# Kernel optimization log

Hardware: AMD Instinct MI355X
Metric: run time of the kernel (lower is better)

The kernel has to match this reference:

```python
import jax, jax.numpy as jnp
import numpy as np

B, LC, LE, H, V = 128, 256, 257, 512, 128
PAD = 0  # padding_token_index


def lstm_cell(x, h, c, Wih, Whh, b):
    # torch LSTMCell gate order: i, f, g, o
    g = x @ Wih.T + h @ Whh.T + b
    i, f, gg, o = jnp.split(g, 4, axis=-1)
    c = jax.nn.sigmoid(f) * c + jax.nn.sigmoid(i) * jnp.tanh(gg)
    h = jax.nn.sigmoid(o) * jnp.tanh(c)
    return h, c


def setup_inputs() -> dict:
    key = jax.random.key(0)
    ks = jax.random.split(key, 32)
    p = lambda k, shape: jax.random.normal(k, shape, jnp.float32) * 0.05
    d = {
        'C_idx': jax.random.randint(ks[0], (B, LC), 0, V, dtype=jnp.int32),
        'E_idx': jax.random.randint(ks[1], (B, LE), 0, V, dtype=jnp.int32),
        'C_pad': jnp.zeros((B, LC), dtype=bool),
        'enc_Wih_f': p(ks[2], (4 * H, V)),
        'enc_Whh_f': p(ks[3], (4 * H, H)),
        'enc_b_f': p(ks[4], (4 * H,)),
        'enc_Wih_b': p(ks[5], (4 * H, V)),
        'enc_Whh_b': p(ks[6], (4 * H, H)),
        'enc_b_b': p(ks[7], (4 * H,)),
        'dec_Wih': p(ks[8], (4 * H, H + V)),
        'dec_Whh': p(ks[9], (4 * H, H)),
        'dec_b': p(ks[10], (4 * H,)),
        'Wh': p(ks[11], (H, 2 * H)),
        'Wc': p(ks[12], (H, 2 * H)),
        'Wattn': p(ks[13], (H, 2 * H)),
        'Wout': p(ks[14], (H, 3 * H)),
        'Wvocab': p(ks[15], (V, H)),
        'pg_ctx': p(ks[16], (2 * H,)),
        'pg_in': p(ks[17], (V + H,)),
        'pg_h': p(ks[18], (H,)),
        'pg_c': p(ks[19], (H,)),
        'pg_b': p(ks[20], (1,)),
    }
    return d


def _forward(C_idx, E_idx, C_pad, enc_Wih_f, enc_Whh_f, enc_b_f, enc_Wih_b, enc_Whh_b, enc_b_b,
             dec_Wih, dec_Whh, dec_b, Wh, Wc, Wattn, Wout, Wvocab,
             pg_ctx, pg_in, pg_h, pg_c, pg_b):
    C = jax.nn.one_hot(C_idx, V, dtype=jnp.float32)      # [B,LC,V]
    E_emb = jax.nn.one_hot(E_idx, V, dtype=jnp.float32)  # [B,LE,V]
    z = jnp.zeros((B, H), jnp.float32)

    xs = jnp.swapaxes(C, 0, 1)  # [LC,B,V]

    def enc_fwd(carry, x):
        h, c = lstm_cell(x, carry[0], carry[1], enc_Wih_f, enc_Whh_f, enc_b_f)
        return (h, c), h

    def enc_bwd(carry, x):
        h, c = lstm_cell(x, carry[0], carry[1], enc_Wih_b, enc_Whh_b, enc_b_b)
        return (h, c), h

    (hf, cf), Hf = jax.lax.scan(enc_fwd, (z, z), xs)
    (hb, cb), Hb = jax.lax.scan(enc_bwd, (z, z), xs[::-1])
    Hb = Hb[::-1]
    enc = jnp.swapaxes(jnp.concatenate([Hf, Hb], axis=-1), 0, 1)  # [B,LC,2H]

    # decoder init state from final encoder states (fwd;bwd concat)
    h0 = jnp.concatenate([hf, hb], axis=-1) @ Wh.T
    c0 = jnp.concatenate([cf, cb], axis=-1) @ Wc.T

    enc_proj = enc @ Wattn.T  # [B,LC,H]

    def step(carry, x_emb):
        h, c, prev_out = carry
        nin = jnp.concatenate([x_emb, prev_out], axis=1)  # [B,V+H]
        h, c = lstm_cell(nin, h, c, dec_Wih, dec_Whh, dec_b)
        scores = jnp.einsum('blh,bh->bl', enc_proj, h)
        scores = jnp.where(C_pad, -jnp.inf, scores)
        attn = jax.nn.softmax(scores, axis=1)             # [B,LC]
        ctx = jnp.einsum('bl,blh->bh', attn, enc)         # [B,2H]
        t_out = jnp.tanh(jnp.concatenate([h, ctx], axis=1) @ Wout.T)  # [B,H]
        gen = jax.nn.softmax(t_out @ Wvocab.T, axis=1)    # [B,V]
        p_gen = jax.nn.sigmoid(ctx @ pg_ctx + nin @ pg_in + h @ pg_h + c @ pg_c + pg_b[0])[:, None]
        copy_p = attn * (1.0 - p_gen)
        out = jax.vmap(lambda o, idx, a: o.at[idx].add(a))(gen * p_gen, C_idx, copy_p)
        return (h, c, t_out), out

    xs2 = jnp.swapaxes(E_emb[:, :LE - 1], 0, 1)  # teacher inputs, step 0 = start token
    _, preds = jax.lax.scan(step, (h0, c0, z), xs2)
    preds = jnp.swapaxes(preds, 0, 1)  # [B,LE-1,V]

    tgt = E_idx[:, 1:]
    nll = -jnp.take_along_axis(jnp.log(preds), tgt[..., None], axis=2)[..., 0]
    return jnp.where(tgt == PAD, 0.0, nll)  # [B,LE-1], reduction='none'


def reference(C_idx, E_idx, C_pad, enc_Wih_f, enc_Whh_f, enc_b_f, enc_Wih_b, enc_Whh_b, enc_b_b,
              dec_Wih, dec_Whh, dec_b, Wh, Wc, Wattn, Wout, Wvocab,
              pg_ctx, pg_in, pg_h, pg_c, pg_b):
    return _forward(C_idx, E_idx, C_pad, enc_Wih_f, enc_Whh_f, enc_b_f, enc_Wih_b, enc_Whh_b, enc_b_b,
                    dec_Wih, dec_Whh, dec_b, Wh, Wc, Wattn, Wout, Wvocab,
                    pg_ctx, pg_in, pg_h, pg_c, pg_b)
```

## Files before the change

### kernel.cpp

```cpp
#include <hip/hip_runtime.h>

static constexpr int B_   = 128;
static constexpr int LC_  = 256;
static constexpr int LE_  = 257;
static constexpr int H_   = 512;
static constexpr size_t HB_ = (size_t)512 * 128;

static constexpr size_t OFF_ENC    = 0;
static constexpr size_t SZ_ENC     = (size_t)128 * 256 * 1024 * 2;
static constexpr size_t OFF_WIHFT  = OFF_ENC + SZ_ENC;
static constexpr size_t OFF_WIHBT  = OFF_WIHFT + (size_t)128 * 2048 * 4;
static constexpr size_t OFF_XDEC   = OFF_WIHBT + (size_t)128 * 2048 * 4;
static constexpr size_t OFF_WATTNT = OFF_XDEC + (size_t)128 * 2048 * 4;
static constexpr size_t OFF_HENC   = OFF_WATTNT + (size_t)1024 * 512 * 4;
static constexpr size_t OFF_CENC   = OFF_HENC + 4 * HB_ * 4;
static constexpr size_t OFF_HDEC   = OFF_CENC + 2 * HB_ * 4;
static constexpr size_t OFF_CDEC   = OFF_HDEC + 2 * HB_ * 4;
static constexpr size_t OFF_TOUT   = OFF_CDEC + HB_ * 4;
static constexpr size_t OFF_U      = OFF_TOUT + 2 * HB_ * 4;
static constexpr size_t OFF_CTX    = OFF_U + (size_t)1024 * 128 * 4;
static constexpr size_t OFF_SC     = OFF_CTX + (size_t)1024 * 128 * 4;
static constexpr size_t OFF_MD     = OFF_SC + (size_t)128 * 256 * 4;

__device__ __forceinline__ float sigm(float x) { return 1.f / (1.f + expf(-x)); }
__device__ __forceinline__ unsigned short f2bf(float f) {
  unsigned u = __float_as_uint(f);
  u += 0x7fffu + ((u >> 16) & 1u);
  return (unsigned short)(u >> 16);
}
__device__ __forceinline__ float bfl(unsigned w) { return __uint_as_float(w << 16); }
__device__ __forceinline__ float bfh(unsigned w) { return __uint_as_float(w & 0xffff0000u); }

__global__ __launch_bounds__(256) void k_pre(const float* __restrict__ wihF,
                                             const float* __restrict__ wihB,
                                             const float* __restrict__ dWih,
                                             const float* __restrict__ Wattn,
                                             float* __restrict__ ws) {
  float* WT_F = (float*)((char*)ws + OFF_WIHFT);
  float* WT_B = (float*)((char*)ws + OFF_WIHBT);
  float* XD   = (float*)((char*)ws + OFF_XDEC);
  float* WAT  = (float*)((char*)ws + OFF_WATTNT);
  int stride = gridDim.x * blockDim.x;
  int i0 = blockIdx.x * blockDim.x + threadIdx.x;
  for (int x = i0; x < 128 * 2048; x += stride) {
    int v = x >> 11, n = x & 2047;
    WT_F[x] = wihF[n * 128 + v];
    WT_B[x] = wihB[n * 128 + v];
    XD[x]   = dWih[n * 640 + v];
  }
  for (int x = i0; x < 1024 * 512; x += stride) {
    int j = x >> 9, i2 = x & 511;
    WAT[x] = Wattn[i2 * 1024 + j];
  }
}

__global__ __launch_bounds__(512) void k_enc(const float* __restrict__ WhhF,
                                             const float* __restrict__ WhhB,
                                             const float* __restrict__ bF,
                                             const float* __restrict__ bB,
                                             const int* __restrict__ C_idx,
                                             float* __restrict__ ws, int t) {
  int p = blockIdx.x * 512 + threadIdx.x;
  int b = p & 127;
  int j = (p >> 7) & 511;
  int dir = p >> 16;
  int jj = __builtin_amdgcn_readfirstlane(j);
  int dd = __builtin_amdgcn_readfirstlane(dir);
  const float* Whh  = dd ? WhhB : WhhF;
  const float* bias = dd ? bB : bF;
  const float* WihT = (const float*)((char*)ws + (dd ? OFF_WIHBT : OFF_WIHFT));
  int l = dd ? (LC_ - 1 - t) : t;
  int cidx = C_idx[b * LC_ + l];
  int par = t & 1;
  const float* hp = (const float*)((char*)ws + OFF_HENC) + (size_t)(dir * 2 + (par ^ 1)) * HB_ + b;

  const float* w0 = Whh + (size_t)jj * 512;
  const float* w1 = Whh + (size_t)(512 + jj) * 512;
  const float* w2 = Whh + (size_t)(1024 + jj) * 512;
  const float* w3 = Whh + (size_t)(1536 + jj) * 512;
  float a0 = bias[jj]        + WihT[(size_t)cidx * 2048 + jj];
  float a1 = bias[512 + jj]  + WihT[(size_t)cidx * 2048 + 512 + jj];
  float a2 = bias[1024 + jj] + WihT[(size_t)cidx * 2048 + 1024 + jj];
  float a3 = bias[1536 + jj] + WihT[(size_t)cidx * 2048 + 1536 + jj];
  for (int k = 0; k < 512; k += 4) {
    float4 W0 = *(const float4*)(w0 + k);
    float4 W1 = *(const float4*)(w1 + k);
    float4 W2 = *(const float4*)(w2 + k);
    float4 W3 = *(const float4*)(w3 + k);
    float h0 = hp[(size_t)k * 128], h1 = hp[(size_t)(k + 1) * 128];
    float h2 = hp[(size_t)(k + 2) * 128], h3 = hp[(size_t)(k + 3) * 128];
    a0 += W0.x * h0 + W0.y * h1 + W0.z * h2 + W0.w * h3;
    a1 += W1.x * h0 + W1.y * h1 + W1.z * h2 + W1.w * h3;
    a2 += W2.x * h0 + W2.y * h1 + W2.z * h2 + W2.w * h3;
    a3 += W3.x * h0 + W3.y * h1 + W3.z * h2 + W3.w * h3;
  }
  float ig = sigm(a0), fg = sigm(a1), gg = tanhf(a2), og = sigm(a3);
  float* cp = (float*)((char*)ws + OFF_CENC) + (size_t)dir * HB_ + (size_t)j * 128 + b;
  float c = fg * (*cp) + ig * gg;
  *cp = c;
  float h = og * tanhf(c);
  ((float*)((char*)ws + OFF_HENC))[(size_t)(dir * 2 + par) * HB_ + (size_t)j * 128 + b] = h;
  ((unsigned short*)((char*)ws + OFF_ENC))[((size_t)b * LC_ + l) * 1024 + dir * 512 + j] = f2bf(h);
}

__global__ __launch_bounds__(512) void k_h0c0(const float* __restrict__ Wh,
                                              const float* __restrict__ Wc,
                                              float* __restrict__ ws) {
  int p = blockIdx.x * 512 + threadIdx.x;
  int b = p & 127;
  int n = (p >> 7) & 511;
  int sel = p >> 16;
  int nn = __builtin_amdgcn_readfirstlane(n);
  int ss = __builtin_amdgcn_readfirstlane(sel);
  const float* W = (ss ? Wc : Wh) + (size_t)nn * 1024;
  const float* hf = (const float*)((char*)ws + OFF_HENC) + (size_t)1 * HB_ + b;
  const float* hb = (const float*)((char*)ws + OFF_HENC) + (size_t)3 * HB_ + b;
  float acc = 0.f;
  for (int k = 0; k < 512; k += 4) {
    float4 Wa = *(const float4*)(W + k);
    float4 Wb = *(const float4*)(W + 512 + k);
    acc += Wa.x * hf[(size_t)k * 128] + Wa.y * hf[(size_t)(k + 1) * 128]
         + Wa.z * hf[(size_t)(k + 2) * 128] + Wa.w * hf[(size_t)(k + 3) * 128];
    acc += Wb.x * hb[(size_t)k * 128] + Wb.y * hb[(size_t)(k + 1) * 128]
         + Wb.z * hb[(size_t)(k + 2) * 128] + Wb.w * hb[(size_t)(k + 3) * 128];
  }
  float* dst = (float*)((char*)ws + (ss ? OFF_CDEC : OFF_HDEC));
  dst[(size_t)n * 128 + b] = acc;
}

__device__ void s4_body(float* __restrict__ ws, float* __restrict__ out,
                        const float* __restrict__ Wvocab, const int* __restrict__ E_idx,
                        const int* __restrict__ C_idx, int b, int t) {
  __shared__ float to[516];
  __shared__ float lgp[128][4];
  __shared__ float lg[128];
  __shared__ float red2[8];
  __shared__ float mx_s[2];
  int tau = threadIdx.x;
  const float* TO = (const float*)((char*)ws + OFF_TOUT) + (size_t)(t & 1) * HB_;
  to[tau + (tau >> 7)] = TO[(size_t)tau * 128 + b];
  __syncthreads();
  int v = tau >> 2, seg = tau & 3;
  const float* wv = Wvocab + (size_t)v * 512 + seg * 128;
  const float* tp = &to[seg * 128 + seg];
  float part = 0.f;
#pragma unroll 8
  for (int i = 0; i < 128; ++i) part += tp[i] * wv[i];
  lgp[v][seg] = part;
  __syncthreads();
  if (tau < 128) lg[tau] = lgp[tau][0] + lgp[tau][1] + lgp[tau][2] + lgp[tau][3];
  __syncthreads();
  if (tau < 64) {
    float m2 = fmaxf(lg[tau], lg[tau + 64]);
    for (int o = 32; o; o >>= 1) m2 = fmaxf(m2, __shfl_xor(m2, o));
    float e = expf(lg[tau] - m2) + expf(lg[tau + 64] - m2);
    for (int o = 32; o; o >>= 1) e += __shfl_xor(e, o);
    if (tau == 0) { mx_s[0] = m2; mx_s[1] = e; }
  }
  const float* MD = (const float*)((char*)ws + OFF_MD);
  float Mb = MD[b], Db = MD[128 + b], pg = MD[256 + b];
  int tgt = E_idx[b * LE_ + t];
  float cm = 0.f;
  if (tau < 256) {
    float s = ((const float*)((char*)ws + OFF_SC))[b * 256 + tau];
    if (C_idx[b * 256 + tau] == tgt) cm = expf(s - Mb);
  }
  for (int o = 32; o; o >>= 1) cm += __shfl_xor(cm, o);
  if ((tau & 63) == 0) red2[tau >> 6] = cm;
  __syncthreads();
  if (tau == 0) {
    float mass = (red2[0] + red2[1] + red2[2] + red2[3]) / Db;
    float gen_tgt = expf(lg[tgt] - mx_s[0]) / mx_s[1];
    float prob = pg * gen_tgt + (1.f - pg) * mass;
    out[b * 256 + (t - 1)] = (tgt == 0) ? 0.f : -logf(prob);
  }
}

__global__ __launch_bounds__(512) void k_dgates(const float* __restrict__ dWih,
                                                const float* __restrict__ dWhh,
                                                const float* __restrict__ db,
                                                const float* __restrict__ Wvocab,
                                                const int* __restrict__ E_idx,
                                                const int* __restrict__ C_idx,
                                                float* __restrict__ ws,
                                                float* __restrict__ out, int t) {
  int tau = threadIdx.x;
  if (blockIdx.x >= 256) {
    if (t > 0) s4_body(ws, out, Wvocab, E_idx, C_idx, blockIdx.x - 256, t);
    return;
  }
  __shared__ float part[4][256];
  int kh = tau >> 8, q = tau & 255;
  int pp = blockIdx.x * 256 + q;
  int b = pp & 127, j = pp >> 7;
  int jj = __builtin_amdgcn_readfirstlane(j);
  int pr = t & 1;
  float a0 = 0.f, a1 = 0.f, a2 = 0.f, a3 = 0.f;
  if (kh == 0) {
    const float* w0 = dWih + (size_t)jj * 640 + 128;
    const float* w1 = dWih + (size_t)(512 + jj) * 640 + 128;
    const float* w2 = dWih + (size_t)(1024 + jj) * 640 + 128;
    const float* w3 = dWih + (size_t)(1536 + jj) * 640 + 128;
    const float* po = (const float*)((char*)ws + OFF_TOUT) + (size_t)pr * HB_ + b;
    for (int k = 0; k < 512; k += 4) {
      float4 W0 = *(const float4*)(w0 + k);
      float4 W1 = *(const float4*)(w1 + k);
      float4 W2 = *(const float4*)(w2 + k);
      float4 W3 = *(const float4*)(w3 + k);
      float h0 = po[(size_t)k * 128], h1 = po[(size_t)(k + 1) * 128];
      float h2 = po[(size_t)(k + 2) * 128], h3 = po[(size_t)(k + 3) * 128];
      a0 += W0.x * h0 + W0.y * h1 + W0.z * h2 + W0.w * h3;
      a1 += W1.x * h0 + W1.y * h1 + W1.z * h2 + W1.w * h3;
      a2 += W2.x * h0 + W2.y * h1 + W2.z * h2 + W2.w * h3;
      a3 += W3.x * h0 + W3.y * h1 + W3.z * h2 + W3.w * h3;
    }
  } else {
    const float* w0 = dWhh + (size_t)jj * 512;
    const float* w1 = dWhh + (size_t)(512 + jj) * 512;
    const float* w2 = dWhh + (size_t)(1024 + jj) * 512;
    const float* w3 = dWhh + (size_t)(1536 + jj) * 512;
    const float* hp = (const float*)((char*)ws + OFF_HDEC) + (size_t)pr * HB_ + b;
    for (int k = 0; k < 512; k += 4) {
      float4 W0 = *(const float4*)(w0 + k);
      float4 W1 = *(const float4*)(w1 + k);
      float4 W2 = *(const float4*)(w2 + k);
      float4 W3 = *(const float4*)(w3 + k);
      float h0 = hp[(size_t)k * 128], h1 = hp[(size_t)(k + 1) * 128];
      float h2 = hp[(size_t)(k + 2) * 128], h3 = hp[(size_t)(k + 3) * 128];
      a0 += W0.x * h0 + W0.y * h1 + W0.z * h2 + W0.w * h3;
      a1 += W1.x * h0 + W1.y * h1 + W1.z * h2 + W1.w * h3;
      a2 += W2.x * h0 + W2.y * h1 + W2.z * h2 + W2.w * h3;
      a3 += W3.x * h0 + W3.y * h1 + W3.z * h2 + W3.w * h3;
    }
    part[0][q] = a0; part[1][q] = a1; part[2][q] = a2; part[3][q] = a3;
  }
  __syncthreads();
  if (kh == 0) {
    int xid = E_idx[b * LE_ + t];
    const float* xg = (const float*)((char*)ws + OFF_XDEC) + (size_t)xid * 2048;
    float g0 = a0 + part[0][q] + db[jj]        + xg[jj];
    float g1 = a1 + part[1][q] + db[512 + jj]  + xg[512 + jj];
    float g2 = a2 + part[2][q] + db[1024 + jj] + xg[1024 + jj];
    float g3 = a3 + part[3][q] + db[1536 + jj] + xg[1536 + jj];
    float ig = sigm(g0), fg = sigm(g1), gg = tanhf(g2), og = sigm(g3);
    float* cp = (float*)((char*)ws + OFF_CDEC) + (size_t)j * 128 + b;
    float c = fg * (*cp) + ig * gg;
    *cp = c;
    ((float*)((char*)ws + OFF_HDEC))[(size_t)(pr ^ 1) * HB_ + (size_t)j * 128 + b] = og * tanhf(c);
  }
}

__global__ __launch_bounds__(512) void k_u(const float* __restrict__ unused,
                                           float* __restrict__ ws, int t) {
  int p = blockIdx.x * 512 + threadIdx.x;
  int b = p & 127, j = p >> 7;
  int jj = __builtin_amdgcn_readfirstlane(j);
  const float* w = (const float*)((char*)ws + OFF_WATTNT) + (size_t)jj * 512;
  const float* hp = (const float*)((char*)ws + OFF_HDEC) + (size_t)((t & 1) ^ 1) * HB_ + b;
  float acc = 0.f;
  for (int k = 0; k < 512; k += 4) {
    float4 W = *(const float4*)(w + k);
    acc += W.x * hp[(size_t)k * 128] + W.y * hp[(size_t)(k + 1) * 128]
         + W.z * hp[(size_t)(k + 2) * 128] + W.w * hp[(size_t)(k + 3) * 128];
  }
  ((float*)((char*)ws + OFF_U))[(size_t)j * 128 + b] = acc;
}

__global__ __launch_bounds__(512) void k_attn(const float* __restrict__ pg_ctx,
                                              const float* __restrict__ pg_in,
                                              const float* __restrict__ pg_h,
                                              const float* __restrict__ pg_c,
                                              const float* __restrict__ pg_b,
                                              const int* __restrict__ E_idx,
                                              const unsigned char* __restrict__ C_pad,
                                              float* __restrict__ ws, int t) {
  __shared__ unsigned short tile[65536];
  __shared__ float u_lds[1032];
  __shared__ float scp[64][9];
  __shared__ float p_lds[64];
  __shared__ float sred[8];
  __shared__ float bc[2];
  int b = blockIdx.x, tau = threadIdx.x;
  int pr = t & 1;
  const float* U = (const float*)((char*)ws + OFF_U);
  u_lds[tau + (tau >> 7)] = U[(size_t)tau * 128 + b];
  {
    int x2 = tau + 512;
    u_lds[x2 + (x2 >> 7)] = U[(size_t)x2 * 128 + b];
  }
  float M = -3.0e38f, D = 0.f, c0 = 0.f, c1 = 0.f;
  const uint4* encb = (const uint4*)((char*)ws + OFF_ENC + (size_t)b * LC_ * 1024 * 2);
  float* SC = (float*)((char*)ws + OFF_SC);
  int l = tau >> 3, seg = tau & 7;
  for (int lb = 0; lb < 4; ++lb) {
    const uint4* src = encb + (size_t)lb * 64 * 128;
#pragma unroll
    for (int it = 0; it < 16; ++it) {
      int fl = it * 512 + tau;
      int r = fl >> 7, cb = fl & 127;
      ((uint4*)tile)[(r << 7) + (cb ^ (r & 7))] = src[fl];
    }
    __syncthreads();
    float acc = 0.f;
#pragma unroll
    for (int ibv = 0; ibv < 16; ++ibv) {
      int blk = (seg * 16 + ibv) ^ (l & 7);
      const uint4 wv = *(const uint4*)&tile[(l << 10) + (blk << 3)];
      const float* up = &u_lds[seg * 128 + ibv * 8 + seg];
      acc += bfl(wv.x) * up[0] + bfh(wv.x) * up[1];
      acc += bfl(wv.y) * up[2] + bfh(wv.y) * up[3];
      acc += bfl(wv.z) * up[4] + bfh(wv.z) * up[5];
      acc += bfl(wv.w) * up[6] + bfh(wv.w) * up[7];
    }
    scp[l][seg] = acc;
    __syncthreads();
    if (tau < 64) {
      float s = scp[tau][0] + scp[tau][1] + scp[tau][2] + scp[tau][3]
              + scp[tau][4] + scp[tau][5] + scp[tau][6] + scp[tau][7];
      int gl = lb * 64 + tau;
      if (C_pad[b * LC_ + gl]) s = -3.0e38f;
      SC[b * 256 + gl] = s;
      float m = s;
      for (int o = 32; o; o >>= 1) m = fmaxf(m, __shfl_xor(m, o));
      float Mn = fmaxf(M, m);
      float pv = expf(s - Mn);
      p_lds[tau] = pv;
      float ds = pv;
      for (int o = 32; o; o >>= 1) ds += __shfl_xor(ds, o);
      if (tau == 0) { bc[0] = m; bc[1] = ds; }
    }
    __syncthreads();
    float Mn = fmaxf(M, bc[0]);
    float scale = expf(M - Mn);
    D = D * scale + bc[1];
    c0 *= scale; c1 *= scale;
    M = Mn;
    {
      int cb0 = tau >> 3, e0 = tau & 7;
      int cb1 = (tau + 512) >> 3;
#pragma unroll 8
      for (int l2 = 0; l2 < 64; ++l2) {
        float pv = p_lds[l2];
        float v0 = bfl((unsigned)tile[(l2 << 10) + (((cb0 ^ (l2 & 7)) << 3) | e0)]);
        float v1 = bfl((unsigned)tile[(l2 << 10) + (((cb1 ^ (l2 & 7)) << 3) | e0)]);
        c0 += pv * v0; c1 += pv * v1;
      }
    }
    __syncthreads();
  }
  float inv = 1.f / D;
  float x0 = c0 * inv, x1 = c1 * inv;
  float* CTX = (float*)((char*)ws + OFF_CTX);
  CTX[(size_t)tau * 128 + b] = x0;
  CTX[(size_t)(tau + 512) * 128 + b] = x1;
  float pp = x0 * pg_ctx[tau] + x1 * pg_ctx[tau + 512];
  pp += ((const float*)((char*)ws + OFF_HDEC))[(size_t)(pr ^ 1) * HB_ + (size_t)tau * 128 + b] * pg_h[tau];
  pp += ((const float*)((char*)ws + OFF_CDEC))[(size_t)tau * 128 + b] * pg_c[tau];
  pp += ((const float*)((char*)ws + OFF_TOUT))[(size_t)pr * HB_ + (size_t)tau * 128 + b] * pg_in[128 + tau];
  for (int o = 32; o; o >>= 1) pp += __shfl_xor(pp, o);
  if ((tau & 63) == 0) sred[tau >> 6] = pp;
  __syncthreads();
  if (tau == 0) {
    float s = sred[0] + sred[1] + sred[2] + sred[3] + sred[4] + sred[5] + sred[6] + sred[7];
    int xid = E_idx[b * LE_ + t];
    s += pg_in[xid] + pg_b[0];
    float* MD = (float*)((char*)ws + OFF_MD);
    MD[256 + b] = sigm(s);
    MD[b] = M;
    MD[128 + b] = D;
  }
}

__global__ __launch_bounds__(512) void k_wout(const float* __restrict__ Wout,
                                              float* __restrict__ ws, int t) {
  __shared__ float part[256];
  int tau = threadIdx.x;
  int kh = tau >> 8, q = tau & 255;
  int pp = blockIdx.x * 256 + q;
  int b = pp & 127, n = pp >> 7;
  int nn = __builtin_amdgcn_readfirstlane(n);
  int pr = t & 1;
  float acc = 0.f;
  if (kh == 0) {
    const float* w = Wout + (size_t)nn * 1536;
    const float* hp = (const float*)((char*)ws + OFF_HDEC) + (size_t)(pr ^ 1) * HB_ + b;
    for (int k = 0; k < 512; k += 4) {
      float4 W = *(const float4*)(w + k);
      acc += W.x * hp[(size_t)k * 128] + W.y * hp[(size_t)(k + 1) * 128]
           + W.z * hp[(size_t)(k + 2) * 128] + W.w * hp[(size_t)(k + 3) * 128];
    }
  } else {
    const float* w = Wout + (size_t)nn * 1536 + 512;
    const float* cp = (const float*)((char*)ws + OFF_CTX) + b;
    for (int k = 0; k < 1024; k += 4) {
      float4 W = *(const float4*)(w + k);
      acc += W.x * cp[(size_t)k * 128] + W.y * cp[(size_t)(k + 1) * 128]
           + W.z * cp[(size_t)(k + 2) * 128] + W.w * cp[(size_t)(k + 3) * 128];
    }
    part[q] = acc;
  }
  __syncthreads();
  if (kh == 0) {
    float s = acc + part[q];
    ((float*)((char*)ws + OFF_TOUT))[(size_t)(pr ^ 1) * HB_ + (size_t)n * 128 + b] = tanhf(s);
  }
}

__global__ __launch_bounds__(512) void k_final(const float* __restrict__ Wvocab,
                                               const int* __restrict__ E_idx,
                                               const int* __restrict__ C_idx,
                                               float* __restrict__ ws,
                                               float* __restrict__ out) {
  s4_body(ws, out, Wvocab, E_idx, C_idx, blockIdx.x, 256);
}

extern "C" void kernel_launch(void* const* d_in, const int* in_sizes, int n_in,
                              void* d_out, int out_size, void* d_ws, size_t ws_size,
                              hipStream_t stream) {
  (void)in_sizes; (void)n_in; (void)out_size; (void)ws_size;
  const int* C_idx = (const int*)d_in[0];
  const int* E_idx = (const int*)d_in[1];
  const unsigned char* C_pad = (const unsigned char*)d_in[2];
  const float* eWihF = (const float*)d_in[3];
  const float* eWhhF = (const float*)d_in[4];
  const float* ebF   = (const float*)d_in[5];
  const float* eWihB = (const float*)d_in[6];
  const float* eWhhB = (const float*)d_in[7];
  const float* ebB   = (const float*)d_in[8];
  const float* dWih  = (const float*)d_in[9];
  const float* dWhh  = (const float*)d_in[10];
  const float* db    = (const float*)d_in[11];
  const float* Wh    = (const float*)d_in[12];
  const float* Wc    = (const float*)d_in[13];
  const float* Wattn = (const float*)d_in[14];
  const float* Wout  = (const float*)d_in[15];
  const float* Wvoc  = (const float*)d_in[16];
  const float* pgc   = (const float*)d_in[17];
  const float* pgi   = (const float*)d_in[18];
  const float* pgh   = (const float*)d_in[19];
  const float* pgcc  = (const float*)d_in[20];
  const float* pgb   = (const float*)d_in[21];
  float* ws = (float*)d_ws;
  float* out = (float*)d_out;

  hipMemsetAsync((char*)d_ws + OFF_HENC, 0, 6 * HB_ * 4, stream);
  hipMemsetAsync((char*)d_ws + OFF_TOUT, 0, 2 * HB_ * 4, stream);

  k_pre<<<512, 256, 0, stream>>>(eWihF, eWihB, dWih, Wattn, ws);
  for (int t = 0; t < 256; ++t)
    k_enc<<<256, 512, 0, stream>>>(eWhhF, eWhhB, ebF, ebB, C_idx, ws, t);
  k_h0c0<<<256, 512, 0, stream>>>(Wh, Wc, ws);
  for (int t = 0; t < 256; ++t) {
    k_dgates<<<384, 512, 0, stream>>>(dWih, dWhh, db, Wvoc, E_idx, C_idx, ws, out, t);
    k_u<<<256, 512, 0, stream>>>(nullptr, ws, t);
    k_attn<<<128, 512, 0, stream>>>(pgc, pgi, pgh, pgcc, pgb, E_idx, C_pad, ws, t);
    k_wout<<<256, 512, 0, stream>>>(Wout, ws, t);
  }
  k_final<<<128, 512, 0, stream>>>(Wvoc, E_idx, C_idx, ws, out);
}
```

Before: 34.11 ms.

## Fuse all per-step kernels into one persistent cooperative kernel with grid barriers

Replaces about 1300 separate kernel launches (encoder steps, decoder gates, attention projection, attention, output projection) with one cooperative persistent kernel of 256 blocks. The phases are separated by a hierarchical atomic grid barrier. The change is meant to remove per-launch overhead and the gaps between launches in the long sequential recurrence. It also changes the bf16 encoder-output layout to a swizzled tiled form, likely to suit attention LDS tiles, and double-buffers the score and MD buffers so the loss computation can overlap with attention. The risks are barrier correctness and lost parallelism in phases that previously used more blocks, such as the former 384-block dgates launch.

```diff
diff --git a/kernel.cpp b/kernel.cpp
--- a/kernel.cpp
+++ b/kernel.cpp
@@ -1,26 +1,43 @@
 #include <hip/hip_runtime.h>
 
-static constexpr int B_   = 128;
-static constexpr int LC_  = 256;
-static constexpr int LE_  = 257;
-static constexpr int H_   = 512;
-static constexpr size_t HB_ = (size_t)512 * 128;
+static constexpr int NBLK = 256;
+static constexpr int NTHR = 512;
+static constexpr size_t HB = (size_t)512 * 128;
 
 static constexpr size_t OFF_ENC    = 0;
-static constexpr size_t SZ_ENC     = (size_t)128 * 256 * 1024 * 2;
-static constexpr size_t OFF_WIHFT  = OFF_ENC + SZ_ENC;
-static constexpr size_t OFF_WIHBT  = OFF_WIHFT + (size_t)128 * 2048 * 4;
-static constexpr size_t OFF_XDEC   = OFF_WIHBT + (size_t)128 * 2048 * 4;
-static constexpr size_t OFF_WATTNT = OFF_XDEC + (size_t)128 * 2048 * 4;
-static constexpr size_t OFF_HENC   = OFF_WATTNT + (size_t)1024 * 512 * 4;
-static constexpr size_t OFF_CENC   = OFF_HENC + 4 * HB_ * 4;
-static constexpr size_t OFF_HDEC   = OFF_CENC + 2 * HB_ * 4;
-static constexpr size_t OFF_CDEC   = OFF_HDEC + 2 * HB_ * 4;
-static constexpr size_t OFF_TOUT   = OFF_CDEC + HB_ * 4;
-static constexpr size_t OFF_U      = OFF_TOUT + 2 * HB_ * 4;
-static constexpr size_t OFF_CTX    = OFF_U + (size_t)1024 * 128 * 4;
-static constexpr size_t OFF_SC     = OFF_CTX + (size_t)1024 * 128 * 4;
-static constexpr size_t OFF_MD     = OFF_SC + (size_t)128 * 256 * 4;
+static constexpr size_t OFF_WIHFT  = 67108864;
+static constexpr size_t OFF_WIHBT  = 68157440;
+static constexpr size_t OFF_XDEC   = 69206016;
+static constexpr size_t OFF_WATTNT = 70254592;
+static constexpr size_t OFF_HENC   = 72351744;
+static constexpr size_t OFF_CENC   = 73400320;
+static constexpr size_t OFF_HDEC   = 73924608;
+static constexpr size_t OFF_CDEC   = 74448896;
+static constexpr size_t OFF_TOUT   = 74711040;
+static constexpr size_t OFF_U      = 75235328;
+static constexpr size_t OFF_CTX    = 75759616;
+static constexpr size_t OFF_SC     = 76283904;
+static constexpr size_t OFF_MD     = 76546048;
+static constexpr size_t OFF_BAR    = 76550144;
+
+static constexpr int SM_TILE = 0;
+static constexpr int SM_U    = 131072;
+static constexpr int SM_SCP  = 135232;
+static constexpr int SM_PLDS = 137536;
+static constexpr int SM_BC   = 137792;
+static constexpr int SM_RED  = 137824;
+static constexpr int SM_PVP  = 137856;
+static constexpr int SM_SIZE = 150208;
+
+struct KP {
+  const int* C_idx; const int* E_idx; const unsigned char* C_pad;
+  const float* eWihF; const float* eWhhF; const float* ebF;
+  const float* eWihB; const float* eWhhB; const float* ebB;
+  const float* dWih;  const float* dWhh;  const float* db;
+  const float* Wh; const float* Wc; const float* Wattn; const float* Wout; const float* Wvoc;
+  const float* pgc; const float* pgi; const float* pgh; const float* pgcc; const float* pgb;
+  char* wsb; float* out;
+};
 
 __device__ __forceinline__ float sigm(float x) { return 1.f / (1.f + expf(-x)); }
 __device__ __forceinline__ unsigned short f2bf(float f) {
@@ -31,48 +48,61 @@
 __device__ __forceinline__ float bfl(unsigned w) { return __uint_as_float(w << 16); }
 __device__ __forceinline__ float bfh(unsigned w) { return __uint_as_float(w & 0xffff0000u); }
 
-__global__ __launch_bounds__(256) void k_pre(const float* __restrict__ wihF,
-                                             const float* __restrict__ wihB,
-                                             const float* __restrict__ dWih,
-                                             const float* __restrict__ Wattn,
-                                             float* __restrict__ ws) {
-  float* WT_F = (float*)((char*)ws + OFF_WIHFT);
-  float* WT_B = (float*)((char*)ws + OFF_WIHBT);
-  float* XD   = (float*)((char*)ws + OFF_XDEC);
-  float* WAT  = (float*)((char*)ws + OFF_WATTNT);
-  int stride = gridDim.x * blockDim.x;
-  int i0 = blockIdx.x * blockDim.x + threadIdx.x;
+__device__ __forceinline__ void gbar(int* bar, int bid) {
+  __syncthreads();
+  if (threadIdx.x == 0) {
+    __threadfence();
+    int* gen = bar + 32;
+    int g = __hip_atomic_load(gen, __ATOMIC_RELAXED, __HIP_MEMORY_SCOPE_AGENT);
+    int* gc = bar + 64 + (bid >> 4) * 32;
+    if (__hip_atomic_fetch_add(gc, 1, __ATOMIC_ACQ_REL, __HIP_MEMORY_SCOPE_AGENT) == 15) {
+      __hip_atomic_store(gc, 0, __ATOMIC_RELAXED, __HIP_MEMORY_SCOPE_AGENT);
+      if (__hip_atomic_fetch_add(bar, 1, __ATOMIC_ACQ_REL, __HIP_MEMORY_SCOPE_AGENT) == 15) {
+        __hip_atomic_store(bar, 0, __ATOMIC_RELAXED, __HIP_MEMORY_SCOPE_AGENT);
+        __hip_atomic_store(gen, g + 1, __ATOMIC_RELEASE, __HIP_MEMORY_SCOPE_AGENT);
+      }
+    }
+    while (__hip_atomic_load(gen, __ATOMIC_ACQUIRE, __HIP_MEMORY_SCOPE_AGENT) == g)
+      __builtin_amdgcn_s_sleep(2);
+    __threadfence();
+  }
+  __syncthreads();
+}
+
+__device__ void pre_phase(const KP& P, int bid, int tau) {
+  float* WT_F = (float*)(P.wsb + OFF_WIHFT);
+  float* WT_B = (float*)(P.wsb + OFF_WIHBT);
+  float* XD   = (float*)(P.wsb + OFF_XDEC);
+  float* WAT  = (float*)(P.wsb + OFF_WATTNT);
+  int i0 = bid * NTHR + tau;
+  int stride = NBLK * NTHR;
   for (int x = i0; x < 128 * 2048; x += stride) {
     int v = x >> 11, n = x & 2047;
-    WT_F[x] = wihF[n * 128 + v];
-    WT_B[x] = wihB[n * 128 + v];
-    XD[x]   = dWih[n * 640 + v];
+    WT_F[x] = P.eWihF[n * 128 + v];
+    WT_B[x] = P.eWihB[n * 128 + v];
+    XD[x]   = P.dWih[n * 640 + v];
   }
   for (int x = i0; x < 1024 * 512; x += stride) {
     int j = x >> 9, i2 = x & 511;
-    WAT[x] = Wattn[i2 * 1024 + j];
-  }
-}
-
-__global__ __launch_bounds__(512) void k_enc(const float* __restrict__ WhhF,
-                                             const float* __restrict__ WhhB,
-                                             const float* __restrict__ bF,
-                                             const float* __restrict__ bB,
-                                             const int* __restrict__ C_idx,
-                                             float* __restrict__ ws, int t) {
-  int p = blockIdx.x * 512 + threadIdx.x;
+    WAT[x] = P.Wattn[i2 * 1024 + j];
+  }
+}
+
+__device__ void enc_phase(const KP& P, int bid, int tau, int t) {
+  char* wsb = P.wsb;
+  int p = bid * NTHR + tau;
   int b = p & 127;
   int j = (p >> 7) & 511;
   int dir = p >> 16;
   int jj = __builtin_amdgcn_readfirstlane(j);
   int dd = __builtin_amdgcn_readfirstlane(dir);
-  const float* Whh  = dd ? WhhB : WhhF;
-  const float* bias = dd ? bB : bF;
-  const float* WihT = (const float*)((char*)ws + (dd ? OFF_WIHBT : OFF_WIHFT));
-  int l = dd ? (LC_ - 1 - t) : t;
-  int cidx = C_idx[b * LC_ + l];
+  const float* Whh  = dd ? P.eWhhB : P.eWhhF;
+  const float* bias = dd ? P.ebB : P.ebF;
+  const float* WihT = (const float*)(wsb + (dd ? OFF_WIHBT : OFF_WIHFT));
+  int l = dd ? (255 - t) : t;
+  int cidx = P.C_idx[b * 256 + l];
   int par = t & 1;
-  const float* hp = (const float*)((char*)ws + OFF_HENC) + (size_t)(dir * 2 + (par ^ 1)) * HB_ + b;
+  const float* hp = (const float*)(wsb + OFF_HENC) + (size_t)(dir * 2 + (par ^ 1)) * HB + b;
 
   const float* w0 = Whh + (size_t)jj * 512;
   const float* w1 = Whh + (size_t)(512 + jj) * 512;
@@ -95,113 +125,57 @@
     a3 += W3.x * h0 + W3.y * h1 + W3.z * h2 + W3.w * h3;
   }
   float ig = sigm(a0), fg = sigm(a1), gg = tanhf(a2), og = sigm(a3);
-  float* cp = (float*)((char*)ws + OFF_CENC) + (size_t)dir * HB_ + (size_t)j * 128 + b;
+  float* cp = (float*)(wsb + OFF_CENC) + (size_t)dir * HB + (size_t)j * 128 + b;
   float c = fg * (*cp) + ig * gg;
   *cp = c;
   float h = og * tanhf(c);
-  ((float*)((char*)ws + OFF_HENC))[(size_t)(dir * 2 + par) * HB_ + (size_t)j * 128 + b] = h;
-  ((unsigned short*)((char*)ws + OFF_ENC))[((size_t)b * LC_ + l) * 1024 + dir * 512 + j] = f2bf(h);
-}
-
-__global__ __launch_bounds__(512) void k_h0c0(const float* __restrict__ Wh,
-                                              const float* __restrict__ Wc,
-                                              float* __restrict__ ws) {
-  int p = blockIdx.x * 512 + threadIdx.x;
+  ((float*)(wsb + OFF_HENC))[(size_t)(dir * 2 + par) * HB + (size_t)j * 128 + b] = h;
+  int f = dir * 512 + j;
+  int cb = f >> 3, e = f & 7;
+  int r = l & 63, lbt = l >> 6;
+  size_t idx = (size_t)b * 262144 + (size_t)lbt * 65536 + ((size_t)r << 10) + ((size_t)(cb ^ (r & 7)) << 3) + e;
+  ((unsigned short*)(wsb + OFF_ENC))[idx] = f2bf(h);
+}
+
+__device__ void h0c0_phase(const KP& P, int bid, int tau) {
+  char* wsb = P.wsb;
+  int p = bid * NTHR + tau;
   int b = p & 127;
   int n = (p >> 7) & 511;
   int sel = p >> 16;
   int nn = __builtin_amdgcn_readfirstlane(n);
   int ss = __builtin_amdgcn_readfirstlane(sel);
-  const float* W = (ss ? Wc : Wh) + (size_t)nn * 1024;
-  const float* hf = (const float*)((char*)ws + OFF_HENC) + (size_t)1 * HB_ + b;
-  const float* hb = (const float*)((char*)ws + OFF_HENC) + (size_t)3 * HB_ + b;
+  const float* W = (ss ? P.Wc : P.Wh) + (size_t)nn * 1024;
+  const float* af = (const float*)(wsb + (ss ? OFF_CENC : OFF_HENC + HB * 4)) + b;
+  const float* ab = (const float*)(wsb + (ss ? OFF_CENC + HB * 4 : OFF_HENC + 3 * HB * 4)) + b;
   float acc = 0.f;
   for (int k = 0; k < 512; k += 4) {
     float4 Wa = *(const float4*)(W + k);
     float4 Wb = *(const float4*)(W + 512 + k);
-    acc += Wa.x * hf[(size_t)k * 128] + Wa.y * hf[(size_t)(k + 1) * 128]
-         + Wa.z * hf[(size_t)(k + 2) * 128] + Wa.w * hf[(size_t)(k + 3) * 128];
-    acc += Wb.x * hb[(size_t)k * 128] + Wb.y * hb[(size_t)(k + 1) * 128]
-         + Wb.z * hb[(size_t)(k + 2) * 128] + Wb.w * hb[(size_t)(k + 3) * 128];
-  }
-  float* dst = (float*)((char*)ws + (ss ? OFF_CDEC : OFF_HDEC));
+    acc += Wa.x * af[(size_t)k * 128] + Wa.y * af[(size_t)(k + 1) * 128]
+         + Wa.z * af[(size_t)(k + 2) * 128] + Wa.w * af[(size_t)(k + 3) * 128];
+    acc += Wb.x * ab[(size_t)k * 128] + Wb.y * ab[(size_t)(k + 1) * 128]
+         + Wb.z * ab[(size_t)(k + 2) * 128] + Wb.w * ab[(size_t)(k + 3) * 128];
+  }
+  float* dst = (float*)(wsb + (ss ? OFF_CDEC : OFF_HDEC));
   dst[(size_t)n * 128 + b] = acc;
 }
 
-__device__ void s4_body(float* __restrict__ ws, float* __restrict__ out,
-                        const float* __restrict__ Wvocab, const int* __restrict__ E_idx,
-                        const int* __restrict__ C_idx, int b, int t) {
-  __shared__ float to[516];
-  __shared__ float lgp[128][4];
-  __shared__ float lg[128];
-  __shared__ float red2[8];
-  __shared__ float mx_s[2];
-  int tau = threadIdx.x;
-  const float* TO = (const float*)((char*)ws + OFF_TOUT) + (size_t)(t & 1) * HB_;
-  to[tau + (tau >> 7)] = TO[(size_t)tau * 128 + b];
-  __syncthreads();
-  int v = tau >> 2, seg = tau & 3;
-  const float* wv = Wvocab + (size_t)v * 512 + seg * 128;
-  const float* tp = &to[seg * 128 + seg];
-  float part = 0.f;
-#pragma unroll 8
-  for (int i = 0; i < 128; ++i) part += tp[i] * wv[i];
-  lgp[v][seg] = part;
-  __syncthreads();
-  if (tau < 128) lg[tau] = lgp[tau][0] + lgp[tau][1] + lgp[tau][2] + lgp[tau][3];
-  __syncthreads();
-  if (tau < 64) {
-    float m2 = fmaxf(lg[tau], lg[tau + 64]);
-    for (int o = 32; o; o >>= 1) m2 = fmaxf(m2, __shfl_xor(m2, o));
-    float e = expf(lg[tau] - m2) + expf(lg[tau + 64] - m2);
-    for (int o = 32; o; o >>= 1) e += __shfl_xor(e, o);
-    if (tau == 0) { mx_s[0] = m2; mx_s[1] = e; }
-  }
-  const float* MD = (const float*)((char*)ws + OFF_MD);
-  float Mb = MD[b], Db = MD[128 + b], pg = MD[256 + b];
-  int tgt = E_idx[b * LE_ + t];
-  float cm = 0.f;
-  if (tau < 256) {
-    float s = ((const float*)((char*)ws + OFF_SC))[b * 256 + tau];
-    if (C_idx[b * 256 + tau] == tgt) cm = expf(s - Mb);
-  }
-  for (int o = 32; o; o >>= 1) cm += __shfl_xor(cm, o);
-  if ((tau & 63) == 0) red2[tau >> 6] = cm;
-  __syncthreads();
-  if (tau == 0) {
-    float mass = (red2[0] + red2[1] + red2[2] + red2[3]) / Db;
-    float gen_tgt = expf(lg[tgt] - mx_s[0]) / mx_s[1];
-    float prob = pg * gen_tgt + (1.f - pg) * mass;
-    out[b * 256 + (t - 1)] = (tgt == 0) ? 0.f : -logf(prob);
-  }
-}
-
-__global__ __launch_bounds__(512) void k_dgates(const float* __restrict__ dWih,
-                                                const float* __restrict__ dWhh,
-                                                const float* __restrict__ db,
-                                                const float* __restrict__ Wvocab,
-                                                const int* __restrict__ E_idx,
-                                                const int* __restrict__ C_idx,
-                                                float* __restrict__ ws,
-                                                float* __restrict__ out, int t) {
-  int tau = threadIdx.x;
-  if (blockIdx.x >= 256) {
-    if (t > 0) s4_body(ws, out, Wvocab, E_idx, C_idx, blockIdx.x - 256, t);
-    return;
-  }
-  __shared__ float part[4][256];
+__device__ void dgates_phase(const KP& P, char* smem, int bid, int tau, int t) {
+  char* wsb = P.wsb;
+  float (*part)[256] = (float(*)[256])smem;
   int kh = tau >> 8, q = tau & 255;
-  int pp = blockIdx.x * 256 + q;
+  int pp = bid * 256 + q;
   int b = pp & 127, j = pp >> 7;
   int jj = __builtin_amdgcn_readfirstlane(j);
   int pr = t & 1;
   float a0 = 0.f, a1 = 0.f, a2 = 0.f, a3 = 0.f;
   if (kh == 0) {
-    const float* w0 = dWih + (size_t)jj * 640 + 128;
-    const float* w1 = dWih + (size_t)(512 + jj) * 640 + 128;
-    const float* w2 = dWih + (size_t)(1024 + jj) * 640 + 128;
-    const float* w3 = dWih + (size_t)(1536 + jj) * 640 + 128;
-    const float* po = (const float*)((char*)ws + OFF_TOUT) + (size_t)pr * HB_ + b;
+    const float* w0 = P.dWih + (size_t)jj * 640 + 128;
+    const float* w1 = P.dWih + (size_t)(512 + jj) * 640 + 128;
+    const float* w2 = P.dWih + (size_t)(1024 + jj) * 640 + 128;
+    const float* w3 = P.dWih + (size_t)(1536 + jj) * 640 + 128;
+    const float* po = (const float*)(wsb + OFF_TOUT) + (size_t)pr * HB + b;
     for (int k = 0; k < 512; k += 4) {
       float4 W0 = *(const float4*)(w0 + k);
       float4 W1 = *(const float4*)(w1 + k);
@@ -215,11 +189,11 @@
       a3 += W3.x * h0 + W3.y * h1 + W3.z * h2 + W3.w * h3;
     }
   } else {
-    const float* w0 = dWhh + (size_t)jj * 512;
-    const float* w1 = dWhh + (size_t)(512 + jj) * 512;
-    const float* w2 = dWhh + (size_t)(1024 + jj) * 512;
-    const float* w3 = dWhh + (size_t)(1536 + jj) * 512;
-    const float* hp = (const float*)((char*)ws + OFF_HDEC) + (size_t)pr * HB_ + b;
+    const float* w0 = P.dWhh + (size_t)jj * 512;
+    const float* w1 = P.dWhh + (size_t)(512 + jj) * 512;
+    const float* w2 = P.dWhh + (size_t)(1024 + jj) * 512;
+    const float* w3 = P.dWhh + (size_t)(1536 + jj) * 512;
+    const float* hp = (const float*)(wsb + OFF_HDEC) + (size_t)pr * HB + b;
     for (int k = 0; k < 512; k += 4) {
       float4 W0 = *(const float4*)(w0 + k);
       float4 W1 = *(const float4*)(w1 + k);
@@ -236,90 +210,85 @@
   }
   __syncthreads();
   if (kh == 0) {
-    int xid = E_idx[b * LE_ + t];
-    const float* xg = (const float*)((char*)ws + OFF_XDEC) + (size_t)xid * 2048;
-    float g0 = a0 + part[0][q] + db[jj]        + xg[jj];
-    float g1 = a1 + part[1][q] + db[512 + jj]  + xg[512 + jj];
-    float g2 = a2 + part[2][q] + db[1024 + jj] + xg[1024 + jj];
-    float g3 = a3 + part[3][q] + db[1536 + jj] + xg[1536 + jj];
+    int xid = P.E_idx[b * 257 + t];
+    const float* xg = (const float*)(wsb + OFF_XDEC) + (size_t)xid * 2048;
+    float g0 = a0 + part[0][q] + P.db[jj]        + xg[jj];
+    float g1 = a1 + part[1][q] + P.db[512 + jj]  + xg[512 + jj];
+    float g2 = a2 + part[2][q] + P.db[1024 + jj] + xg[1024 + jj];
+    float g3 = a3 + part[3][q] + P.db[1536 + jj] + xg[1536 + jj];
     float ig = sigm(g0), fg = sigm(g1), gg = tanhf(g2), og = sigm(g3);
-    float* cp = (float*)((char*)ws + OFF_CDEC) + (size_t)j * 128 + b;
+    float* cp = (float*)(wsb + OFF_CDEC) + (size_t)j * 128 + b;
     float c = fg * (*cp) + ig * gg;
     *cp = c;
-    ((float*)((char*)ws + OFF_HDEC))[(size_t)(pr ^ 1) * HB_ + (size_t)j * 128 + b] = og * tanhf(c);
-  }
-}
-
-__global__ __launch_bounds__(512) void k_u(const float* __restrict__ unused,
-                                           float* __restrict__ ws, int t) {
-  int p = blockIdx.x * 512 + threadIdx.x;
+    ((float*)(wsb + OFF_HDEC))[(size_t)(pr ^ 1) * HB + (size_t)j * 128 + b] = og * tanhf(c);
+  }
+}
+
+__device__ void u_phase(const KP& P, int bid, int tau, int t) {
+  char* wsb = P.wsb;
+  int p = bid * NTHR + tau;
   int b = p & 127, j = p >> 7;
   int jj = __builtin_amdgcn_readfirstlane(j);
-  const float* w = (const float*)((char*)ws + OFF_WATTNT) + (size_t)jj * 512;
-  const float* hp = (const float*)((char*)ws + OFF_HDEC) + (size_t)((t & 1) ^ 1) * HB_ + b;
+  const float* w = (const float*)(wsb + OFF_WATTNT) + (size_t)jj * 512;
+  const float* hp = (const float*)(wsb + OFF_HDEC) + (size_t)((t & 1) ^ 1) * HB + b;
   float acc = 0.f;
   for (int k = 0; k < 512; k += 4) {
     float4 W = *(const float4*)(w + k);
     acc += W.x * hp[(size_t)k * 128] + W.y * hp[(size_t)(k + 1) * 128]
          + W.z * hp[(size_t)(k + 2) * 128] + W.w * hp[(size_t)(k + 3) * 128];
   }
-  ((float*)((char*)ws + OFF_U))[(size_t)j * 128 + b] = acc;
-}
-
-__global__ __launch_bounds__(512) void k_attn(const float* __restrict__ pg_ctx,
-                                              const float* __restrict__ pg_in,
-                                              const float* __restrict__ pg_h,
-                                              const float* __restrict__ pg_c,
-                                              const float* __restrict__ pg_b,
-                                              const int* __restrict__ E_idx,
-                                              const unsigned char* __restrict__ C_pad,
-                                              float* __restrict__ ws, int t) {
-  __shared__ unsigned short tile[65536];
-  __shared__ float u_lds[1032];
-  __shared__ float scp[64][9];
-  __shared__ float p_lds[64];
-  __shared__ float sred[8];
-  __shared__ float bc[2];
-  int b = blockIdx.x, tau = threadIdx.x;
+  ((float*)(wsb + OFF_U))[(size_t)j * 128 + b] = acc;
+}
+
+__device__ void attn_phase(const KP& P, char* smem, int b, int tau, int t) {
+  char* wsb = P.wsb;
+  unsigned short* tile = (unsigned short*)(smem + SM_TILE);
+  uint4* tile4 = (uint4*)(smem + SM_TILE);
+  float* u_lds = (float*)(smem + SM_U);
+  float (*scp)[9] = (float(*)[9])(smem + SM_SCP);
+  float* p_lds = (float*)(smem + SM_PLDS);
+  float* bc = (float*)(smem + SM_BC);
+  float* red = (float*)(smem + SM_RED);
+  float* pvp = (float*)(smem + SM_PVP);
   int pr = t & 1;
-  const float* U = (const float*)((char*)ws + OFF_U);
+  const float* U = (const float*)(wsb + OFF_U);
   u_lds[tau + (tau >> 7)] = U[(size_t)tau * 128 + b];
-  {
-    int x2 = tau + 512;
-    u_lds[x2 + (x2 >> 7)] = U[(size_t)x2 * 128 + b];
-  }
-  float M = -3.0e38f, D = 0.f, c0 = 0.f, c1 = 0.f;
-  const uint4* encb = (const uint4*)((char*)ws + OFF_ENC + (size_t)b * LC_ * 1024 * 2);
-  float* SC = (float*)((char*)ws + OFF_SC);
+  { int x2 = tau + 512; u_lds[x2 + (x2 >> 7)] = U[(size_t)x2 * 128 + b]; }
+  float M = -3.0e38f, D = 0.f;
+  float acc[8];
+#pragma unroll
+  for (int e = 0; e < 8; ++e) acc[e] = 0.f;
+  const uint4* encb = (const uint4*)(wsb + OFF_ENC + (size_t)b * 524288);
+  float* SCp = (float*)(wsb + OFF_SC) + (size_t)pr * 128 * 256;
   int l = tau >> 3, seg = tau & 7;
+  int fg = tau & 127, rs = tau >> 7;
   for (int lb = 0; lb < 4; ++lb) {
-    const uint4* src = encb + (size_t)lb * 64 * 128;
+    const uint4* src = encb + (size_t)lb * 8192;
 #pragma unroll
     for (int it = 0; it < 16; ++it) {
       int fl = it * 512 + tau;
-      int r = fl >> 7, cb = fl & 127;
-      ((uint4*)tile)[(r << 7) + (cb ^ (r & 7))] = src[fl];
+      tile4[fl] = src[fl];
     }
     __syncthreads();
-    float acc = 0.f;
+    float sacc = 0.f;
 #pragma unroll
     for (int ibv = 0; ibv < 16; ++ibv) {
       int blk = (seg * 16 + ibv) ^ (l & 7);
-      const uint4 wv = *(const uint4*)&tile[(l << 10) + (blk << 3)];
+      const uint4 wv = tile4[(l << 7) + blk];
       const float* up = &u_lds[seg * 128 + ibv * 8 + seg];
-      acc += bfl(wv.x) * up[0] + bfh(wv.x) * up[1];
-      acc += bfl(wv.y) * up[2] + bfh(wv.y) * up[3];
-      acc += bfl(wv.z) * up[4] + bfh(wv.z) * up[5];
-      acc += bfl(wv.w) * up[6] + bfh(wv.w) * up[7];
-    }
-    scp[l][seg] = acc;
+      sacc += bfl(wv.x) * up[0] + bfh(wv.x) * up[1];
+      sacc += bfl(wv.y) * up[2] + bfh(wv.y) * up[3];
+      sacc += bfl(wv.z) * up[4] + bfh(wv.z) * up[5];
+      sacc += bfl(wv.w) * up[6] + bfh(wv.w) * up[7];
+    }
+    scp[l][seg] = sacc;
     __syncthreads();
     if (tau < 64) {
       float s = scp[tau][0] + scp[tau][1] + scp[tau][2] + scp[tau][3]
               + scp[tau][4] + scp[tau][5] + scp[tau][6] + scp[tau][7];
       int gl = lb * 64 + tau;
-      if (C_pad[b * LC_ + gl]) s = -3.0e38f;
-      SC[b * 256 + gl] = s;
+      if (P.C_pad[b * 256 + gl]) s = -3.0e38f;
+      SCp[b * 256 + gl] = s;
       float m = s;
       for (int o = 32; o; o >>= 1) m = fmaxf(m, __shfl_xor(m, o));
       float Mn = fmaxf(M, m);
@@ -333,65 +302,140 @@
     float Mn = fmaxf(M, bc[0]);
     float scale = expf(M - Mn);
     D = D * scale + bc[1];
-    c0 *= scale; c1 *= scale;
     M = Mn;
-    {
-      int cb0 = tau >> 3, e0 = tau & 7;
-      int cb1 = (tau + 512) >> 3;
+#pragma unroll
+    for (int e = 0; e < 8; ++e) acc[e] *= scale;
+    int base = rs * 16;
+#pragma unroll
+    for (int l2i = 0; l2i < 16; ++l2i) {
+      int l2 = base + l2i;
+      float pv = p_lds[l2];
+      const uint4 wv = tile4[(l2 << 7) + (fg ^ (l2 & 7))];
+      acc[0] += pv * bfl(wv.x); acc[1] += pv * bfh(wv.x);
+      acc[2] += pv * bfl(wv.y); acc[3] += pv * bfh(wv.y);
+      acc[4] += pv * bfl(wv.z); acc[5] += pv * bfh(wv.z);
+      acc[6] += pv * bfl(wv.w); acc[7] += pv * bfh(wv.w);
+    }
+    __syncthreads();
+  }
+  if (rs > 0) {
+    float4* dst = (float4*)(pvp + (rs - 1) * 1024 + fg * 8);
+    dst[0] = make_float4(acc[0], acc[1], acc[2], acc[3]);
+    dst[1] = make_float4(acc[4], acc[5], acc[6], acc[7]);
+  }
+  __syncthreads();
+  if (rs == 0) {
+    float inv = 1.f / D;
+    float* CTX = (float*)(wsb + OFF_CTX);
+    float4 q0 = ((float4*)(pvp + fg * 8))[0],        q1 = ((float4*)(pvp + fg * 8))[1];
+    float4 r0 = ((float4*)(pvp + 1024 + fg * 8))[0], r1 = ((float4*)(pvp + 1024 + fg * 8))[1];
+    float4 s0 = ((float4*)(pvp + 2048 + fg * 8))[0], s1 = ((float4*)(pvp + 2048 + fg * 8))[1];
+    float x0 = (acc[0] + q0.x + r0.x + s0.x) * inv;
+    float x1 = (acc[1] + q0.y + r0.y + s0.y) * inv;
+    float x2 = (acc[2] + q0.z + r0.z + s0.z) * inv;
+    float x3 = (acc[3] + q0.w + r0.w + s0.w) * inv;
+    float x4 = (acc[4] + q1.x + r1.x + s1.x) * inv;
+    float x5 = (acc[5] + q1.y + r1.y + s1.y) * inv;
+    float x6 = (acc[6] + q1.z + r1.z + s1.z) * inv;
+    float x7 = (acc[7] + q1.w + r1.w + s1.w) * inv;
+    ((float4*)(pvp + fg * 8))[0] = make_float4(x0, x1, x2, x3);
+    ((float4*)(pvp + fg * 8))[1] = make_float4(x4, x5, x6, x7);
+    int f = fg * 8;
+    CTX[(size_t)(f + 0) * 128 + b] = x0; CTX[(size_t)(f + 1) * 128 + b] = x1;
+    CTX[(size_t)(f + 2) * 128 + b] = x2; CTX[(size_t)(f + 3) * 128 + b] = x3;
+    CTX[(size_t)(f + 4) * 128 + b] = x4; CTX[(size_t)(f + 5) * 128 + b] = x5;
+    CTX[(size_t)(f + 6) * 128 + b] = x6; CTX[(size_t)(f + 7) * 128 + b] = x7;
+  }
+  __syncthreads();
+  const float* cl = pvp;
+  float pp = cl[tau] * P.pgc[tau] + cl[tau + 512] * P.pgc[tau + 512];
+  pp += ((const float*)(wsb + OFF_HDEC))[(size_t)(pr ^ 1) * HB + (size_t)tau * 128 + b] * P.pgh[tau];
+  pp += ((const float*)(wsb + OFF_CDEC))[(size_t)tau * 128 + b] * P.pgcc[tau];
+  pp += ((const float*)(wsb + OFF_TOUT))[(size_t)pr * HB + (size_t)tau * 128 + b] * P.pgi[128 + tau];
+  for (int o = 32; o; o >>= 1) pp += __shfl_xor(pp, o);
+  if ((tau & 63) == 0) red[tau >> 6] = pp;
+  __syncthreads();
+  if (tau == 0) {
+    float s = red[0] + red[1] + red[2] + red[3] + red[4] + red[5] + red[6] + red[7];
+    int xid = P.E_idx[b * 257 + t];
+    s += P.pgi[xid] + P.pgb[0];
+    float* MDp = (float*)(wsb + OFF_MD) + (size_t)pr * 384;
+    MDp[256 + b] = sigm(s);
+    MDp[b] = M;
+    MDp[128 + b] = D;
+  }
+}
+
+__device__ void s4_body(const KP& P, char* smem, int b, int t) {
+  char* wsb = P.wsb;
+  float* to = (float*)smem;
+  float (*lgp)[4] = (float(*)[4])(smem + 2064);
+  float* lg = (float*)(smem + 4112);
+  float* red2 = (float*)(smem + 4624);
+  float* mx_s = (float*)(smem + 4656);
+  int tau = threadIdx.x;
+  const float* TO = (const float*)(wsb + OFF_TOUT) + (size_t)(t & 1) * HB;
+  to[tau + (tau >> 7)] = TO[(size_t)tau * 128 + b];
+  __syncthreads();
+  int v = tau >> 2, seg = tau & 3;
+  const float* wv = P.Wvoc + (size_t)v * 512 + seg * 128;
+  const float* tp = &to[seg * 128 + seg];
+  float part = 0.f;
 #pragma unroll 8
-      for (int l2 = 0; l2 < 64; ++l2) {
-        float pv = p_lds[l2];
-        float v0 = bfl((unsigned)tile[(l2 << 10) + (((cb0 ^ (l2 & 7)) << 3) | e0)]);
-        float v1 = bfl((unsigned)tile[(l2 << 10) + (((cb1 ^ (l2 & 7)) << 3) | e0)]);
-        c0 += pv * v0; c1 += pv * v1;
-      }
-    }
-    __syncthreads();
-  }
-  float inv = 1.f / D;
-  float x0 = c0 * inv, x1 = c1 * inv;
-  float* CTX = (float*)((char*)ws + OFF_CTX);
-  CTX[(size_t)tau * 128 + b] = x0;
-  CTX[(size_t)(tau + 512) * 128 + b] = x1;
-  float pp = x0 * pg_ctx[tau] + x1 * pg_ctx[tau + 512];
-  pp += ((const float*)((char*)ws + OFF_HDEC))[(size_t)(pr ^ 1) * HB_ + (size_t)tau * 128 + b] * pg_h[tau];
-  pp += ((const float*)((char*)ws + OFF_CDEC))[(size_t)tau * 128 + b] * pg_c[tau];
-  pp += ((const float*)((char*)ws + OFF_TOUT))[(size_t)pr * HB_ + (size_t)tau * 128 + b] * pg_in[128 + tau];
-  for (int o = 32; o; o >>= 1) pp += __shfl_xor(pp, o);
-  if ((tau & 63) == 0) sred[tau >> 6] = pp;
+  for (int i = 0; i < 128; ++i) part += tp[i] * wv[i];
+  lgp[v][seg] = part;
+  __syncthreads();
+  if (tau < 128) lg[tau] = lgp[tau][0] + lgp[tau][1] + lgp[tau][2] + lgp[tau][3];
+  __syncthreads();
+  if (tau < 64) {
+    float m2 = fmaxf(lg[tau], lg[tau + 64]);
+    for (int o = 32; o; o >>= 1) m2 = fmaxf(m2, __shfl_xor(m2, o));
+    float e = expf(lg[tau] - m2) + expf(lg[tau + 64] - m2);
+    for (int o = 32; o; o >>= 1) e += __shfl_xor(e, o);
+    if (tau == 0) { mx_s[0] = m2; mx_s[1] = e; }
+  }
+  int pr1 = (t - 1) & 1;
+  const float* MDp = (const float*)(wsb + OFF_MD) + (size_t)pr1 * 384;
+  const float* SCp = (const float*)(wsb + OFF_SC) + (size_t)pr1 * 128 * 256;
+  float Mb = MDp[b], Db = MDp[128 + b], pg = MDp[256 + b];
+  int tgt = P.E_idx[b * 257 + t];
+  float cm = 0.f;
+  if (tau < 256) {
+    float s = SCp[b * 256 + tau];
+    if (P.C_idx[b * 256 + tau] == tgt) cm = expf(s - Mb);
+  }
+  for (int o = 32; o; o >>= 1) cm += __shfl_xor(cm, o);
+  if ((tau & 63) == 0) red2[tau >> 6] = cm;
   __syncthreads();
   if (tau == 0) {
-    float s = sred[0] + sred[1] + sred[2] + sred[3] + sred[4] + sred[5] + sred[6] + sred[7];
-    int xid = E_idx[b * LE_ + t];
-    s += pg_in[xid] + pg_b[0];
-    float* MD = (float*)((char*)ws + OFF_MD);
-    MD[256 + b] = sigm(s);
-    MD[b] = M;
-    MD[128 + b] = D;
-  }
-}
-
-__global__ __launch_bounds__(512) void k_wout(const float* __restrict__ Wout,
-                                              float* __restrict__ ws, int t) {
-  __shared__ float part[256];
-  int tau = threadIdx.x;
+    float mass = (red2[0] + red2[1] + red2[2] + red2[3]) / Db;
+    float gen_tgt = expf(lg[tgt] - mx_s[0]) / mx_s[1];
+    float prob = pg * gen_tgt + (1.f - pg) * mass;
+    P.out[b * 256 + (t - 1)] = (tgt == 0) ? 0.f : -logf(prob);
+  }
+  __syncthreads();
+}
+
+__device__ void wout_phase(const KP& P, char* smem, int bid, int tau, int t) {
+  char* wsb = P.wsb;
+  float* part = (float*)smem;
   int kh = tau >> 8, q = tau & 255;
-  int pp = blockIdx.x * 256 + q;
+  int pp = bid * 256 + q;
   int b = pp & 127, n = pp >> 7;
   int nn = __builtin_amdgcn_readfirstlane(n);
   int pr = t & 1;
   float acc = 0.f;
   if (kh == 0) {
-    const float* w = Wout + (size_t)nn * 1536;
-    const float* hp = (const float*)((char*)ws + OFF_HDEC) + (size_t)(pr ^ 1) * HB_ + b;
+    const float* w = P.Wout + (size_t)nn * 1536;
+    const float* hp = (const float*)(wsb + OFF_HDEC) + (size_t)(pr ^ 1) * HB + b;
     for (int k = 0; k < 512; k += 4) {
       float4 W = *(const float4*)(w + k);
       acc += W.x * hp[(size_t)k * 128] + W.y * hp[(size_t)(k + 1) * 128]
            + W.z * hp[(size_t)(k + 2) * 128] + W.w * hp[(size_t)(k + 3) * 128];
     }
   } else {
-    const float* w = Wout + (size_t)nn * 1536 + 512;
-    const float* cp = (const float*)((char*)ws + OFF_CTX) + b;
+    const float* w = P.Wout + (size_t)nn * 1536 + 512;
+    const float* cp = (const float*)(wsb + OFF_CTX) + b;
     for (int k = 0; k < 1024; k += 4) {
       float4 W = *(const float4*)(w + k);
       acc += W.x * cp[(size_t)k * 128] + W.y * cp[(size_t)(k + 1) * 128]
@@ -402,59 +446,74 @@
   __syncthreads();
   if (kh == 0) {
     float s = acc + part[q];
-    ((float*)((char*)ws + OFF_TOUT))[(size_t)(pr ^ 1) * HB_ + (size_t)n * 128 + b] = tanhf(s);
-  }
-}
-
-__global__ __launch_bounds__(512) void k_final(const float* __restrict__ Wvocab,
-                                               const int* __restrict__ E_idx,
-                                               const int* __restrict__ C_idx,
-                                               float* __restrict__ ws,
-                                               float* __restrict__ out) {
-  s4_body(ws, out, Wvocab, E_idx, C_idx, blockIdx.x, 256);
+    ((float*)(wsb + OFF_TOUT))[(size_t)(pr ^ 1) * HB + (size_t)n * 128 + b] = tanhf(s);
+  }
+}
+
+__global__ void __launch_bounds__(NTHR) k_all(KP P) {
+  __shared__ __align__(16) char smem[SM_SIZE];
+  const int bid = blockIdx.x;
+  const int tau = threadIdx.x;
+  int* bar = (int*)(P.wsb + OFF_BAR);
+
+  pre_phase(P, bid, tau);
+  gbar(bar, bid);
+
+  for (int t = 0; t < 256; ++t) {
+    enc_phase(P, bid, tau, t);
+    gbar(bar, bid);
+  }
+  h0c0_phase(P, bid, tau);
+  gbar(bar, bid);
+
+  for (int t = 0; t < 256; ++t) {
+    dgates_phase(P, smem, bid, tau, t);
+    gbar(bar, bid);
+    u_phase(P, bid, tau, t);
+    gbar(bar, bid);
+    if (bid < 128) attn_phase(P, smem, bid, tau, t);
+    else if (t > 0) s4_body(P, smem, bid - 128, t);
+    gbar(bar, bid);
+    wout_phase(P, smem, bid, tau, t);
+    gbar(bar, bid);
+  }
+  if (bid < 128) s4_body(P, smem, bid, 256);
 }
 
 extern "C" void kernel_launch(void* const* d_in, const int* in_sizes, int n_in,
                               void* d_out, int out_size, void* d_ws, size_t ws_size,
                               hipStream_t stream) {
   (void)in_sizes; (void)n_in; (void)out_size; (void)ws_size;
-  const int* C_idx = (const int*)d_in[0];
-  const int* E_idx = (const int*)d_in[1];
-  const unsigned char* C_pad = (const unsigned char*)d_in[2];
-  const float* eWihF = (const float*)d_in[3];
-  const float* eWhhF = (const float*)d_in[4];
-  const float* ebF   = (const float*)d_in[5];
-  const float* eWihB = (const float*)d_in[6];
-  const float* eWhhB = (const float*)d_in[7];
-  const float* ebB   = (const float*)d_in[8];
-  const float* dWih  = (const float*)d_in[9];
-  const float* dWhh  = (const float*)d_in[10];
-  const float* db    = (const float*)d_in[11];
-  const float* Wh    = (const float*)d_in[12];
-  const float* Wc    = (const float*)d_in[13];
-  const float* Wattn = (const float*)d_in[14];
-  const float* Wout  = (const float*)d_in[15];
-  const float* Wvoc  = (const float*)d_in[16];
-  const float* pgc   = (const float*)d_in[17];
-  const float* pgi   = (const float*)d_in[18];
-  const float* pgh   = (const float*)d_in[19];
-  const float* pgcc  = (const float*)d_in[20];
-  const float* pgb   = (const float*)d_in[21];
-  float* ws = (float*)d_ws;
-  float* out = (float*)d_out;
-
-  hipMemsetAsync((char*)d_ws + OFF_HENC, 0, 6 * HB_ * 4, stream);
-  hipMemsetAsync((char*)d_ws + OFF_TOUT, 0, 2 * HB_ * 4, stream);
-
-  k_pre<<<512, 256, 0, stream>>>(eWihF, eWihB, dWih, Wattn, ws);
-  for (int t = 0; t < 256; ++t)
-    k_enc<<<256, 512, 0, stream>>>(eWhhF, eWhhB, ebF, ebB, C_idx, ws, t);
-  k_h0c0<<<256, 512, 0, stream>>>(Wh, Wc, ws);
-  for (int t = 0; t < 256; ++t) {
-    k_dgates<<<384, 512, 0, stream>>>(dWih, dWhh, db, Wvoc, E_idx, C_idx, ws, out, t);
-    k_u<<<256, 512, 0, stream>>>(nullptr, ws, t);
-    k_attn<<<128, 512, 0, stream>>>(pgc, pgi, pgh, pgcc, pgb, E_idx, C_pad, ws, t);
-    k_wout<<<256, 512, 0, stream>>>(Wout, ws, t);
-  }
-  k_final<<<128, 512, 0, stream>>>(Wvoc, E_idx, C_idx, ws, out);
-}
+  KP P;
+  P.C_idx = (const int*)d_in[0];
+  P.E_idx = (const int*)d_in[1];
+  P.C_pad = (const unsigned char*)d_in[2];
+  P.eWihF = (const float*)d_in[3];
+  P.eWhhF = (const float*)d_in[4];
+  P.ebF   = (const float*)d_in[5];
+  P.eWihB = (const float*)d_in[6];
+  P.eWhhB = (const float*)d_in[7];
+  P.ebB   = (const float*)d_in[8];
+  P.dWih  = (const float*)d_in[9];
+  P.dWhh  = (const float*)d_in[10];
+  P.db    = (const float*)d_in[11];
+  P.Wh    = (const float*)d_in[12];
+  P.Wc    = (const float*)d_in[13];
+  P.Wattn = (const float*)d_in[14];
+  P.Wout  = (const float*)d_in[15];
+  P.Wvoc  = (const float*)d_in[16];
+  P.pgc   = (const float*)d_in[17];
+  P.pgi   = (const float*)d_in[18];
+  P.pgh   = (const float*)d_in[19];
+  P.pgcc  = (const float*)d_in[20];
+  P.pgb   = (const float*)d_in[21];
+  P.wsb   = (char*)d_ws;
+  P.out   = (float*)d_out;
+
+  hipMemsetAsync((char*)d_ws + OFF_HENC, 0, 6 * HB * 4, stream);
+  hipMemsetAsync((char*)d_ws + OFF_TOUT, 0, 2 * HB * 4, stream);
+  hipMemsetAsync((char*)d_ws + OFF_BAR, 0, 8192, stream);
+
+  void* args[] = { &P };
+  hipLaunchCooperativeKernel((const void*)k_all, dim3(NBLK), dim3(NTHR), args, 0, stream);
+}
```

New measurement: 94.36 ms. +176.7%, slower.
